# Optimization experiments

Measured on AMD Instinct MI355X. Metric: run time of the kernel, lower is better.

The kernel has to match this reference:

```python
import jax, jax.numpy as jnp
import numpy as np

B, H, S, DK = 2, 16, 2048, 128


def setup_inputs() -> dict:
    key = jax.random.key(0)
    kq, kk, kv = jax.random.split(key, 3)
    return {
        "queries": jax.random.normal(kq, (B, H, S, DK), dtype=jnp.float32),
        "keys": jax.random.normal(kk, (B, H, S, DK), dtype=jnp.float32),
        "values": jax.random.normal(kv, (B, H, S, DK), dtype=jnp.float32),
        "d_k": DK,
    }


def reference(queries, keys, values, d_k):
    # scores: [B, H, Sq, Sk] = Q @ K^T / sqrt(d_k)
    scale = 1.0 / np.sqrt(float(d_k)).astype(np.float32)
    scores = jnp.einsum("bhqd,bhkd->bhqk", queries, keys) * scale
    weights = jax.nn.softmax(scores, axis=-1)
    return jnp.einsum("bhqk,bhkd->bhqd", weights, values)
```

## Files before the change

kernel.cpp:

```cpp
#include <hip/hip_runtime.h>
#include <hip/hip_bf16.h>

#define SREF 2048
#define DHEAD 128
#define KVBLK 64
#define NTHREADS 256
#define ATHREADS 512
#define NT (SREF / KVBLK)
#define PSTR 72
#define QSCALE 0.12751743f
#define THRLOG 8.0f

typedef short bf16x8 __attribute__((ext_vector_type(8)));
typedef float f32x4 __attribute__((ext_vector_type(4)));
typedef float f32x16 __attribute__((ext_vector_type(16)));

typedef const __attribute__((address_space(1))) void* gas_t;
typedef __attribute__((address_space(3))) void* las_t;

__device__ __forceinline__ ushort f2bf(float x) {
    unsigned u = __builtin_bit_cast(unsigned, x);
    u += 0x7fffu + ((u >> 16) & 1u);
    return (ushort)(u >> 16);
}

__device__ __forceinline__ float fexp2(float x) {
#if __has_builtin(__builtin_amdgcn_exp2f)
    return __builtin_amdgcn_exp2f(x);
#else
    return exp2f(x);
#endif
}

__device__ __forceinline__ unsigned cvtpk(float lo, float hi) {
    unsigned r;
    asm("v_cvt_pk_bf16_f32 %0, %1, %2" : "=v"(r) : "v"(lo), "v"(hi));
    return r;
}

__global__ __launch_bounds__(NTHREADS) void preconv_kernel(
    const float* __restrict__ K, const float* __restrict__ V,
    ushort* __restrict__ Kb, ushort* __restrict__ VTb)
{
    __shared__ ushort T[DHEAD * PSTR];
    const int t  = threadIdx.x;
    const int bh = blockIdx.y;
    const int s0 = blockIdx.x * 64;
    const size_t base = (size_t)bh * SREF * DHEAD;

    const float* kb = K + base + (size_t)s0 * DHEAD;
    ushort* kout = Kb + base + (size_t)s0 * DHEAD;
    #pragma unroll
    for (int i = 0; i < 8; ++i) {
        int idx = t + i * NTHREADS;
        float4 f = *(const float4*)(kb + idx * 4);
        ushort4 h; h.x = f2bf(f.x); h.y = f2bf(f.y); h.z = f2bf(f.z); h.w = f2bf(f.w);
        *(ushort4*)(kout + idx * 4) = h;
    }

    const float* vb = V + base + (size_t)s0 * DHEAD;
    #pragma unroll
    for (int i = 0; i < 8; ++i) {
        const int key = (t & 31) + 32 * (i & 1);
        const int d4  = (t >> 5) + 8 * (i >> 1);
        float4 f = *(const float4*)(vb + key * DHEAD + d4 * 4);
        T[(d4 * 4 + 0) * PSTR + key] = f2bf(f.x);
        T[(d4 * 4 + 1) * PSTR + key] = f2bf(f.y);
        T[(d4 * 4 + 2) * PSTR + key] = f2bf(f.z);
        T[(d4 * 4 + 3) * PSTR + key] = f2bf(f.w);
    }
    __syncthreads();

    ushort* vt = VTb + (size_t)bh * DHEAD * SREF + s0;
    #pragma unroll
    for (int i = 0; i < 4; ++i) {
        int idx = t + i * NTHREADS;
        int d = idx >> 3;
        int c = (idx & 7) * 8;
        bf16x8 v = *(const bf16x8*)&T[d * PSTR + c];
        *(bf16x8*)(vt + (size_t)d * SREF + c) = v;
    }
}

__device__ __forceinline__ void softmax_step(
    f32x16& s0, f32x16& s1, float& mrun, float& lsumh,
    f32x16* acc, bf16x8* pa)
{
    float m0[8];
    #pragma unroll
    for (int i = 0; i < 8; ++i)
        m0[i] = fmaxf(fmaxf(s0[i], s0[i + 8]), fmaxf(s1[i], s1[i + 8]));
    float pmax = fmaxf(fmaxf(fmaxf(m0[0], m0[1]), fmaxf(m0[2], m0[3])),
                       fmaxf(fmaxf(m0[4], m0[5]), fmaxf(m0[6], m0[7])));
    pmax = fmaxf(pmax, __shfl_xor(pmax, 32));

    if (!__all(pmax <= mrun + THRLOG)) {
        const float mnew  = fmaxf(mrun, pmax);
        const float alpha = fexp2(mrun - mnew);
        mrun = mnew;
        lsumh *= alpha;
        #pragma unroll
        for (int db = 0; db < 4; ++db)
            #pragma unroll
            for (int i = 0; i < 16; ++i) acc[db][i] *= alpha;
    }

    float r0 = 0.f, r1 = 0.f, r2 = 0.f, r3 = 0.f;
    #pragma unroll
    for (int i = 0; i < 16; i += 4) {
        s0[i]   = fexp2(s0[i]   - mrun); r0 += s0[i];
        s0[i+1] = fexp2(s0[i+1] - mrun); r1 += s0[i+1];
        s0[i+2] = fexp2(s0[i+2] - mrun); r2 += s0[i+2];
        s0[i+3] = fexp2(s0[i+3] - mrun); r3 += s0[i+3];
    }
    #pragma unroll
    for (int i = 0; i < 16; i += 4) {
        s1[i]   = fexp2(s1[i]   - mrun); r0 += s1[i];
        s1[i+1] = fexp2(s1[i+1] - mrun); r1 += s1[i+1];
        s1[i+2] = fexp2(s1[i+2] - mrun); r2 += s1[i+2];
        s1[i+3] = fexp2(s1[i+3] - mrun); r3 += s1[i+3];
    }
    lsumh += (r0 + r1) + (r2 + r3);

    #pragma unroll
    for (int kb = 0; kb < 2; ++kb) {
        #pragma unroll
        for (int c = 0; c < 2; ++c) {
            unsigned x0, x1, y0, y1;
            if (kb == 0) {
                x0 = cvtpk(s0[8*c+0], s0[8*c+1]); x1 = cvtpk(s0[8*c+2], s0[8*c+3]);
                y0 = cvtpk(s0[8*c+4], s0[8*c+5]); y1 = cvtpk(s0[8*c+6], s0[8*c+7]);
            } else {
                x0 = cvtpk(s1[8*c+0], s1[8*c+1]); x1 = cvtpk(s1[8*c+2], s1[8*c+3]);
                y0 = cvtpk(s1[8*c+4], s1[8*c+5]); y1 = cvtpk(s1[8*c+6], s1[8*c+7]);
            }
            asm volatile("v_permlane32_swap_b32 %0, %1" : "+v"(x0), "+v"(y0));
            asm volatile("v_permlane32_swap_b32 %0, %1" : "+v"(x1), "+v"(y1));
            union { unsigned u[4]; bf16x8 v; } U;
            U.u[0] = x0; U.u[1] = x1; U.u[2] = y0; U.u[3] = y1;
            pa[kb * 2 + c] = U.v;
        }
    }
}

__global__ __launch_bounds__(ATHREADS, 2) void attn_fwd_kernel(
    const float* __restrict__ Q, const ushort* __restrict__ Kb,
    const ushort* __restrict__ VTb, float* __restrict__ O)
{
    __shared__ __align__(16) char smem[65536];

    const int t    = threadIdx.x;
    const int lane = t & 63;
    const int wv   = t >> 6;
    const int g    = wv >> 2;
    const int hi   = lane >> 5;
    const int q5   = lane & 31;
    const int sw   = (q5 & 15) << 4;

    const int bh = blockIdx.x;
    const int q0 = blockIdx.y * 256;
    const size_t base = (size_t)bh * SREF * DHEAD;

    bf16x8 qf[8];
    {
        const float* qrow = Q + base + (size_t)(q0 + wv * 32 + q5) * DHEAD;
        #pragma unroll
        for (int dk = 0; dk < 8; ++dk) {
            const int d0 = dk * 16 + hi * 8;
            float4 a = *(const float4*)(qrow + d0);
            float4 b = *(const float4*)(qrow + d0 + 4);
            bf16x8 f;
            f[0] = (short)f2bf(a.x * QSCALE); f[1] = (short)f2bf(a.y * QSCALE);
            f[2] = (short)f2bf(a.z * QSCALE); f[3] = (short)f2bf(a.w * QSCALE);
            f[4] = (short)f2bf(b.x * QSCALE); f[5] = (short)f2bf(b.y * QSCALE);
            f[6] = (short)f2bf(b.z * QSCALE); f[7] = (short)f2bf(b.w * QSCALE);
            qf[dk] = f;
        }
    }

    const char* ksrcb = (const char*)(Kb + base);
    const char* vsrcb = (const char*)(VTb + (size_t)bh * DHEAD * SREF);

    const int kread = q5 * 256 + ((hi * 16) ^ sw);
    const int vread = q5 * 256 + ((hi * 16) ^ sw);

#define STAGE_K(tt) do {                                                        \
    const char* kt_ = ksrcb + (size_t)(tt) * 16384;                             \
    _Pragma("unroll")                                                           \
    for (int i_ = 0; i_ < 2; ++i_) {                                            \
        int L_ = t * 16 + i_ * 8192;                                            \
        int r_ = L_ >> 8;                                                       \
        __builtin_amdgcn_global_load_lds(                                       \
            (gas_t)(const void*)(kt_ + (L_ ^ ((r_ & 15) << 4))),                \
            (las_t)(void*)(smem + ((tt) & 1) * 16384 + L_), 16, 0, 0);          \
    }                                                                           \
} while (0)

#define STAGE_V(tt) do {                                                        \
    const char* vt_ = vsrcb + (size_t)(tt) * 128;                               \
    _Pragma("unroll")                                                           \
    for (int i_ = 0; i_ < 2; ++i_) {                                            \
        int L_ = t * 16 + i_ * 8192;                                            \
        int r_ = L_ >> 8;                                                       \
        int offp_ = (L_ & 255) ^ ((r_ & 15) << 4);                              \
        int d_ = r_ + 64 * (offp_ >> 7);                                        \
        __builtin_amdgcn_global_load_lds(                                       \
            (gas_t)(const void*)(vt_ + (size_t)d_ * (SREF * 2) + (offp_ & 127)),\
            (las_t)(void*)(smem + 32768 + ((tt) & 1) * 16384 + L_), 16, 0, 0);  \
    }                                                                           \
} while (0)

#define QK(tt) do {                                                             \
    const int kO_ = ((tt) & 1) * 16384;                                         \
    _Pragma("unroll")                                                           \
    for (int i_ = 0; i_ < 16; ++i_) { s0[i_] = 0.f; s1[i_] = 0.f; }             \
    __builtin_amdgcn_s_setprio(1);                                              \
    _Pragma("unroll")                                                           \
    for (int dk_ = 0; dk_ < 8; ++dk_) {                                         \
        const int off_ = kread ^ (dk_ << 5);                                    \
        bf16x8 kf0 = *(const bf16x8*)(smem + kO_ + off_);                       \
        s0 = __builtin_amdgcn_mfma_f32_32x32x16_bf16(kf0, qf[dk_], s0, 0, 0, 0);\
        bf16x8 kf1 = *(const bf16x8*)(smem + kO_ + 8192 + off_);                \
        s1 = __builtin_amdgcn_mfma_f32_32x32x16_bf16(kf1, qf[dk_], s1, 0, 0, 0);\
    }                                                                           \
    __builtin_amdgcn_s_setprio(0);                                              \
} while (0)

#define PV(tt) do {                                                             \
    const int vO_ = 32768 + ((tt) & 1) * 16384;                                 \
    __builtin_amdgcn_s_setprio(1);                                              \
    _Pragma("unroll")                                                           \
    for (int db_ = 0; db_ < 4; ++db_) {                                         \
        const int vb_ = vread + (db_ & 1) * 8192;                               \
        _Pragma("unroll")                                                       \
        for (int ks_ = 0; ks_ < 4; ++ks_) {                                     \
            bf16x8 vf = *(const bf16x8*)(smem + vO_ +                           \
                (vb_ ^ (ks_ << 5) ^ ((db_ >> 1) << 7)));                        \
            acc[db_] = __builtin_amdgcn_mfma_f32_32x32x16_bf16(vf, pa[ks_], acc[db_], 0, 0, 0); \
        }                                                                       \
    }                                                                           \
    __builtin_amdgcn_s_setprio(0);                                              \
} while (0)

#define BAR() do { __builtin_amdgcn_s_barrier(); __builtin_amdgcn_sched_barrier(0); } while (0)

    float mrun = -1e30f, lsumh = 0.0f;
    f32x16 acc[4];
    #pragma unroll
    for (int db = 0; db < 4; ++db)
        #pragma unroll
        for (int i = 0; i < 16; ++i) acc[db][i] = 0.0f;

    f32x16 s0, s1;
    bf16x8 pa[4];

    STAGE_K(0);
    asm volatile("s_waitcnt vmcnt(0)" ::: "memory");
    BAR();

    STAGE_K(1);
    STAGE_V(0);
    if (g == 0) { QK(0); }
    BAR();
    if (g == 0) { softmax_step(s0, s1, mrun, lsumh, acc, pa); }
    else        { QK(0); }
    asm volatile("s_waitcnt vmcnt(0)" ::: "memory");
    BAR();

    #pragma unroll 1
    for (int tt = 1; tt < NT; ++tt) {
        if (tt + 1 < NT) STAGE_K(tt + 1);
        STAGE_V(tt);
        if (g == 0) { PV(tt - 1); QK(tt); }
        else        { softmax_step(s0, s1, mrun, lsumh, acc, pa); }
        BAR();
        if (g == 0) { softmax_step(s0, s1, mrun, lsumh, acc, pa); }
        else        { PV(tt - 1); QK(tt); }
        asm volatile("s_waitcnt vmcnt(0)" ::: "memory");
        BAR();
    }

    if (g == 0) { PV(NT - 1); }
    else        { softmax_step(s0, s1, mrun, lsumh, acc, pa); }
    BAR();
    if (g == 1) { PV(NT - 1); }

    __syncthreads();
    const float lsum = lsumh + __shfl_xor(lsumh, 32);
    const float inv  = 1.0f / lsum;

    #pragma unroll
    for (int round = 0; round < 3; ++round) {
        if (wv / 3 == round) {
            const int eb = (wv % 3) * 16896;
            #pragma unroll
            for (int db = 0; db < 4; ++db) {
                #pragma unroll
                for (int c = 0; c < 4; ++c) {
                    f32x4 v;
                    v[0] = acc[db][4*c+0] * inv;
                    v[1] = acc[db][4*c+1] * inv;
                    v[2] = acc[db][4*c+2] * inv;
                    v[3] = acc[db][4*c+3] * inv;
                    *(f32x4*)(smem + eb + q5 * 528 + db * 128 + c * 32 + hi * 16) = v;
                }
            }
            #pragma unroll
            for (int i = 0; i < 16; ++i) {
                const int flat  = lane + i * 64;
                const int row   = flat >> 5;
                const int chunk = flat & 31;
                f32x4 v = *(const f32x4*)(smem + eb + row * 528 + chunk * 16);
                *(f32x4*)(O + base + (size_t)(q0 + wv * 32 + row) * DHEAD + chunk * 4) = v;
            }
        }
        __syncthreads();
    }
#undef STAGE_K
#undef STAGE_V
#undef QK
#undef PV
#undef BAR
}

__global__ __launch_bounds__(NTHREADS) void attn_fwd_fallback(
    const float* __restrict__ Q, const float* __restrict__ K,
    const float* __restrict__ V, float* __restrict__ O)
{
    __shared__ ushort Ksh[64 * 136];
    __shared__ ushort Vsh[DHEAD * 72];
    __shared__ ushort Psh[4][16 * PSTR];

    const int t    = threadIdx.x;
    const int lane = t & 63;
    const int wv   = t >> 6;
    const int lq   = lane & 15;
    const int kh   = lane >> 4;

    const int bh = blockIdx.y;
    const int q0 = blockIdx.x * 64;
    const size_t base = (size_t)bh * SREF * DHEAD;

    const float scale = 0.08838834764831845f;
    bf16x8 qf[4];
    {
        const float* qrow = Q + base + (size_t)(q0 + wv * 16 + lq) * DHEAD;
        #pragma unroll
        for (int kk = 0; kk < 4; ++kk) {
            const int d0 = kk * 32 + kh * 8;
            float4 a = *(const float4*)(qrow + d0);
            float4 b = *(const float4*)(qrow + d0 + 4);
            bf16x8 f;
            f[0] = (short)f2bf(a.x * scale); f[1] = (short)f2bf(a.y * scale);
            f[2] = (short)f2bf(a.z * scale); f[3] = (short)f2bf(a.w * scale);
            f[4] = (short)f2bf(b.x * scale); f[5] = (short)f2bf(b.y * scale);
            f[6] = (short)f2bf(b.z * scale); f[7] = (short)f2bf(b.w * scale);
            qf[kk] = f;
        }
    }

    float mrun[4], lrun[4];
    f32x4 acc_o[8];
    #pragma unroll
    for (int r = 0; r < 4; ++r) { mrun[r] = -1e30f; lrun[r] = 0.0f; }
    #pragma unroll
    for (int db = 0; db < 8; ++db) acc_o[db] = (f32x4){0.f, 0.f, 0.f, 0.f};

    for (int kv0 = 0; kv0 < SREF; kv0 += 64) {
        __syncthreads();
        const float* kbase = K + base + (size_t)kv0 * DHEAD;
        #pragma unroll
        for (int i = 0; i < 8; ++i) {
            const int idx = t + i * NTHREADS;
            const int row = idx >> 5;
            const int c4  = idx & 31;
            float4 f = *(const float4*)(kbase + row * DHEAD + c4 * 4);
            ushort4 h;
            h.x = f2bf(f.x); h.y = f2bf(f.y); h.z = f2bf(f.z); h.w = f2bf(f.w);
            *(ushort4*)&Ksh[row * 136 + c4 * 4] = h;
        }
        const float* vbase = V + base + (size_t)kv0 * DHEAD;
        #pragma unroll
        for (int i = 0; i < 8; ++i) {
            const int key = (t & 31) + 32 * (i & 1);
            const int d4  = (t >> 5) + 8 * (i >> 1);
            float4 f = *(const float4*)(vbase + key * DHEAD + d4 * 4);
            Vsh[(d4 * 4 + 0) * 72 + key] = f2bf(f.x);
            Vsh[(d4 * 4 + 1) * 72 + key] = f2bf(f.y);
            Vsh[(d4 * 4 + 2) * 72 + key] = f2bf(f.z);
            Vsh[(d4 * 4 + 3) * 72 + key] = f2bf(f.w);
        }
        __syncthreads();

        f32x4 accs[4];
        #pragma unroll
        for (int nb = 0; nb < 4; ++nb) accs[nb] = (f32x4){0.f, 0.f, 0.f, 0.f};
        #pragma unroll
        for (int kk = 0; kk < 4; ++kk) {
            #pragma unroll
            for (int nb = 0; nb < 4; ++nb) {
                bf16x8 kf = *(const bf16x8*)&Ksh[(nb * 16 + lq) * 136 + kk * 32 + kh * 8];
                accs[nb] = __builtin_amdgcn_mfma_f32_16x16x32_bf16(qf[kk], kf, accs[nb], 0, 0, 0);
            }
        }

        float ps[4][4];
        #pragma unroll
        for (int r = 0; r < 4; ++r) {
            float v = fmaxf(fmaxf(accs[0][r], accs[1][r]), fmaxf(accs[2][r], accs[3][r]));
            #pragma unroll
            for (int mk = 1; mk < 16; mk <<= 1) v = fmaxf(v, __shfl_xor(v, mk));
            const float mnew  = fmaxf(mrun[r], v);
            const float alpha = __expf(mrun[r] - mnew);
            mrun[r] = mnew;
            float rs = 0.0f;
            #pragma unroll
            for (int nb = 0; nb < 4; ++nb) {
                const float p = __expf(accs[nb][r] - mnew);
                ps[nb][r] = p;
                rs += p;
            }
            #pragma unroll
            for (int mk = 1; mk < 16; mk <<= 1) rs += __shfl_xor(rs, mk);
            lrun[r] = lrun[r] * alpha + rs;
            #pragma unroll
            for (int db = 0; db < 8; ++db) acc_o[db][r] *= alpha;
        }

        #pragma unroll
        for (int nb = 0; nb < 4; ++nb)
            #pragma unroll
            for (int r = 0; r < 4; ++r)
                Psh[wv][(kh * 4 + r) * PSTR + nb * 16 + lq] = f2bf(ps[nb][r]);

        #pragma unroll
        for (int ks = 0; ks < 2; ++ks) {
            bf16x8 pa = *(const bf16x8*)&Psh[wv][lq * PSTR + ks * 32 + kh * 8];
            #pragma unroll
            for (int db = 0; db < 8; ++db) {
                bf16x8 vf = *(const bf16x8*)&Vsh[(db * 16 + lq) * 72 + ks * 32 + kh * 8];
                acc_o[db] = __builtin_amdgcn_mfma_f32_16x16x32_bf16(pa, vf, acc_o[db], 0, 0, 0);
            }
        }
    }

    #pragma unroll
    for (int r = 0; r < 4; ++r) {
        const float inv = 1.0f / lrun[r];
        float* orow = O + base + (size_t)(q0 + wv * 16 + kh * 4 + r) * DHEAD;
        #pragma unroll
        for (int db = 0; db < 8; ++db)
            orow[db * 16 + lq] = acc_o[db][r] * inv;
    }
}

extern "C" void kernel_launch(void* const* d_in, const int* in_sizes, int n_in,
                              void* d_out, int out_size, void* d_ws, size_t ws_size,
                              hipStream_t stream) {
    const float* Q = (const float*)d_in[0];
    const float* K = (const float*)d_in[1];
    const float* V = (const float*)d_in[2];
    float* O = (float*)d_out;
    const int BH = in_sizes[0] / (SREF * DHEAD);
    const size_t nel = (size_t)BH * SREF * DHEAD;

    if (ws_size >= 2 * nel * sizeof(ushort)) {
        ushort* Kb  = (ushort*)d_ws;
        ushort* VTb = Kb + nel;
        preconv_kernel<<<dim3(SREF / 64, BH), NTHREADS, 0, stream>>>(K, V, Kb, VTb);
        attn_fwd_kernel<<<dim3(BH, SREF / 256), ATHREADS, 0, stream>>>(Q, Kb, VTb, O);
    } else {
        attn_fwd_fallback<<<dim3(SREF / 64, BH), NTHREADS, 0, stream>>>(Q, K, V, O);
    }
}
```

Before: 98.59 us.

## Process two query tiles per wave with 256 threads, dropping ping-pong wave groups

Replaces the 512-thread design, where two 4-wave groups alternate QK/PV and softmax between barriers, with 4 waves that each own 64 query rows split into two 32-row tiles (A/B). Each K/V fragment read from LDS now feeds two MFMAs, halving LDS reads per FLOP. K and V staging is merged into one double-buffered stage with a partial vmcnt wait. The trade-off is the loss of cross-group overlap between softmax and matrix work, fewer waves per CU, and roughly double the accumulator register pressure.

```diff
diff --git a/kernel.cpp b/kernel.cpp
--- a/kernel.cpp
+++ b/kernel.cpp
@@ -5,7 +5,6 @@
 #define DHEAD 128
 #define KVBLK 64
 #define NTHREADS 256
-#define ATHREADS 512
 #define NT (SREF / KVBLK)
 #define PSTR 72
 #define QSCALE 0.12751743f
@@ -143,7 +142,7 @@
     }
 }
 
-__global__ __launch_bounds__(ATHREADS, 2) void attn_fwd_kernel(
+__global__ __launch_bounds__(NTHREADS, 1) void attn_fwd_kernel(
     const float* __restrict__ Q, const ushort* __restrict__ Kb,
     const ushort* __restrict__ VTb, float* __restrict__ O)
 {
@@ -152,7 +151,6 @@
     const int t    = threadIdx.x;
     const int lane = t & 63;
     const int wv   = t >> 6;
-    const int g    = wv >> 2;
     const int hi   = lane >> 5;
     const int q5   = lane & 31;
     const int sw   = (q5 & 15) << 4;
@@ -161,20 +159,29 @@
     const int q0 = blockIdx.y * 256;
     const size_t base = (size_t)bh * SREF * DHEAD;
 
-    bf16x8 qf[8];
+    bf16x8 qfA[8], qfB[8];
     {
-        const float* qrow = Q + base + (size_t)(q0 + wv * 32 + q5) * DHEAD;
+        const float* qrowA = Q + base + (size_t)(q0 + wv * 64 + q5) * DHEAD;
+        const float* qrowB = qrowA + 32 * DHEAD;
         #pragma unroll
         for (int dk = 0; dk < 8; ++dk) {
             const int d0 = dk * 16 + hi * 8;
-            float4 a = *(const float4*)(qrow + d0);
-            float4 b = *(const float4*)(qrow + d0 + 4);
+            float4 a = *(const float4*)(qrowA + d0);
+            float4 b = *(const float4*)(qrowA + d0 + 4);
             bf16x8 f;
             f[0] = (short)f2bf(a.x * QSCALE); f[1] = (short)f2bf(a.y * QSCALE);
             f[2] = (short)f2bf(a.z * QSCALE); f[3] = (short)f2bf(a.w * QSCALE);
             f[4] = (short)f2bf(b.x * QSCALE); f[5] = (short)f2bf(b.y * QSCALE);
             f[6] = (short)f2bf(b.z * QSCALE); f[7] = (short)f2bf(b.w * QSCALE);
-            qf[dk] = f;
+            qfA[dk] = f;
+            float4 c = *(const float4*)(qrowB + d0);
+            float4 d = *(const float4*)(qrowB + d0 + 4);
+            bf16x8 g;
+            g[0] = (short)f2bf(c.x * QSCALE); g[1] = (short)f2bf(c.y * QSCALE);
+            g[2] = (short)f2bf(c.z * QSCALE); g[3] = (short)f2bf(c.w * QSCALE);
+            g[4] = (short)f2bf(d.x * QSCALE); g[5] = (short)f2bf(d.y * QSCALE);
+            g[6] = (short)f2bf(d.z * QSCALE); g[7] = (short)f2bf(d.w * QSCALE);
+            qfB[dk] = g;
         }
     }
 
@@ -182,25 +189,22 @@
     const char* vsrcb = (const char*)(VTb + (size_t)bh * DHEAD * SREF);
 
     const int kread = q5 * 256 + ((hi * 16) ^ sw);
-    const int vread = q5 * 256 + ((hi * 16) ^ sw);
-
-#define STAGE_K(tt) do {                                                        \
+    const int vread = kread;
+
+#define STAGE(tt) do {                                                          \
     const char* kt_ = ksrcb + (size_t)(tt) * 16384;                             \
+    const char* vt_ = vsrcb + (size_t)(tt) * 128;                               \
     _Pragma("unroll")                                                           \
-    for (int i_ = 0; i_ < 2; ++i_) {                                            \
-        int L_ = t * 16 + i_ * 8192;                                            \
+    for (int i_ = 0; i_ < 4; ++i_) {                                            \
+        int L_ = t * 16 + i_ * 4096;                                            \
         int r_ = L_ >> 8;                                                       \
         __builtin_amdgcn_global_load_lds(                                       \
             (gas_t)(const void*)(kt_ + (L_ ^ ((r_ & 15) << 4))),                \
             (las_t)(void*)(smem + ((tt) & 1) * 16384 + L_), 16, 0, 0);          \
     }                                                                           \
-} while (0)
-
-#define STAGE_V(tt) do {                                                        \
-    const char* vt_ = vsrcb + (size_t)(tt) * 128;                               \
     _Pragma("unroll")                                                           \
-    for (int i_ = 0; i_ < 2; ++i_) {                                            \
-        int L_ = t * 16 + i_ * 8192;                                            \
+    for (int i_ = 0; i_ < 4; ++i_) {                                            \
+        int L_ = t * 16 + i_ * 4096;                                            \
         int r_ = L_ >> 8;                                                       \
         int offp_ = (L_ & 255) ^ ((r_ & 15) << 4);                              \
         int d_ = r_ + 64 * (offp_ >> 7);                                        \
@@ -210,117 +214,107 @@
     }                                                                           \
 } while (0)
 
-#define QK(tt) do {                                                             \
-    const int kO_ = ((tt) & 1) * 16384;                                         \
-    _Pragma("unroll")                                                           \
-    for (int i_ = 0; i_ < 16; ++i_) { s0[i_] = 0.f; s1[i_] = 0.f; }             \
-    __builtin_amdgcn_s_setprio(1);                                              \
-    _Pragma("unroll")                                                           \
-    for (int dk_ = 0; dk_ < 8; ++dk_) {                                         \
-        const int off_ = kread ^ (dk_ << 5);                                    \
-        bf16x8 kf0 = *(const bf16x8*)(smem + kO_ + off_);                       \
-        s0 = __builtin_amdgcn_mfma_f32_32x32x16_bf16(kf0, qf[dk_], s0, 0, 0, 0);\
-        bf16x8 kf1 = *(const bf16x8*)(smem + kO_ + 8192 + off_);                \
-        s1 = __builtin_amdgcn_mfma_f32_32x32x16_bf16(kf1, qf[dk_], s1, 0, 0, 0);\
-    }                                                                           \
-    __builtin_amdgcn_s_setprio(0);                                              \
-} while (0)
-
-#define PV(tt) do {                                                             \
-    const int vO_ = 32768 + ((tt) & 1) * 16384;                                 \
-    __builtin_amdgcn_s_setprio(1);                                              \
-    _Pragma("unroll")                                                           \
-    for (int db_ = 0; db_ < 4; ++db_) {                                         \
-        const int vb_ = vread + (db_ & 1) * 8192;                               \
-        _Pragma("unroll")                                                       \
-        for (int ks_ = 0; ks_ < 4; ++ks_) {                                     \
-            bf16x8 vf = *(const bf16x8*)(smem + vO_ +                           \
-                (vb_ ^ (ks_ << 5) ^ ((db_ >> 1) << 7)));                        \
-            acc[db_] = __builtin_amdgcn_mfma_f32_32x32x16_bf16(vf, pa[ks_], acc[db_], 0, 0, 0); \
-        }                                                                       \
-    }                                                                           \
-    __builtin_amdgcn_s_setprio(0);                                              \
-} while (0)
-
-#define BAR() do { __builtin_amdgcn_s_barrier(); __builtin_amdgcn_sched_barrier(0); } while (0)
-
-    float mrun = -1e30f, lsumh = 0.0f;
-    f32x16 acc[4];
+    float mrunA = -1e30f, lsumA = 0.0f;
+    float mrunB = -1e30f, lsumB = 0.0f;
+    f32x16 accA[4], accB[4];
     #pragma unroll
     for (int db = 0; db < 4; ++db)
         #pragma unroll
-        for (int i = 0; i < 16; ++i) acc[db][i] = 0.0f;
-
-    f32x16 s0, s1;
-    bf16x8 pa[4];
-
-    STAGE_K(0);
-    asm volatile("s_waitcnt vmcnt(0)" ::: "memory");
-    BAR();
-
-    STAGE_K(1);
-    STAGE_V(0);
-    if (g == 0) { QK(0); }
-    BAR();
-    if (g == 0) { softmax_step(s0, s1, mrun, lsumh, acc, pa); }
-    else        { QK(0); }
-    asm volatile("s_waitcnt vmcnt(0)" ::: "memory");
-    BAR();
+        for (int i = 0; i < 16; ++i) { accA[db][i] = 0.0f; accB[db][i] = 0.0f; }
+
+    f32x16 sA0, sA1, sB0, sB1;
+    bf16x8 paA[4], paB[4];
+
+    STAGE(0);
 
     #pragma unroll 1
-    for (int tt = 1; tt < NT; ++tt) {
-        if (tt + 1 < NT) STAGE_K(tt + 1);
-        STAGE_V(tt);
-        if (g == 0) { PV(tt - 1); QK(tt); }
-        else        { softmax_step(s0, s1, mrun, lsumh, acc, pa); }
-        BAR();
-        if (g == 0) { softmax_step(s0, s1, mrun, lsumh, acc, pa); }
-        else        { PV(tt - 1); QK(tt); }
-        asm volatile("s_waitcnt vmcnt(0)" ::: "memory");
-        BAR();
-    }
-
-    if (g == 0) { PV(NT - 1); }
-    else        { softmax_step(s0, s1, mrun, lsumh, acc, pa); }
-    BAR();
-    if (g == 1) { PV(NT - 1); }
+    for (int tt = 0; tt < NT; ++tt) {
+        if (tt + 1 < NT) {
+            STAGE(tt + 1);
+            asm volatile("s_waitcnt vmcnt(8)" ::: "memory");
+        } else {
+            asm volatile("s_waitcnt vmcnt(0)" ::: "memory");
+        }
+        __builtin_amdgcn_s_barrier();
+        __builtin_amdgcn_sched_barrier(0);
+
+        const int kO = ((tt) & 1) * 16384;
+        const int vO = 32768 + ((tt) & 1) * 16384;
+
+        #pragma unroll
+        for (int i = 0; i < 16; ++i) { sA0[i] = 0.f; sA1[i] = 0.f; sB0[i] = 0.f; sB1[i] = 0.f; }
+        #pragma unroll
+        for (int dk = 0; dk < 8; ++dk) {
+            const int off = kread ^ (dk << 5);
+            bf16x8 kf0 = *(const bf16x8*)(smem + kO + off);
+            bf16x8 kf1 = *(const bf16x8*)(smem + kO + 8192 + off);
+            sA0 = __builtin_amdgcn_mfma_f32_32x32x16_bf16(kf0, qfA[dk], sA0, 0, 0, 0);
+            sB0 = __builtin_amdgcn_mfma_f32_32x32x16_bf16(kf0, qfB[dk], sB0, 0, 0, 0);
+            sA1 = __builtin_amdgcn_mfma_f32_32x32x16_bf16(kf1, qfA[dk], sA1, 0, 0, 0);
+            sB1 = __builtin_amdgcn_mfma_f32_32x32x16_bf16(kf1, qfB[dk], sB1, 0, 0, 0);
+        }
+
+        softmax_step(sA0, sA1, mrunA, lsumA, accA, paA);
+        softmax_step(sB0, sB1, mrunB, lsumB, accB, paB);
+
+        #pragma unroll
+        for (int db = 0; db < 4; ++db) {
+            const int vb = vread + (db & 1) * 8192;
+            #pragma unroll
+            for (int ks = 0; ks < 4; ++ks) {
+                bf16x8 vf = *(const bf16x8*)(smem + vO +
+                    (vb ^ (ks << 5) ^ ((db >> 1) << 7)));
+                accA[db] = __builtin_amdgcn_mfma_f32_32x32x16_bf16(vf, paA[ks], accA[db], 0, 0, 0);
+                accB[db] = __builtin_amdgcn_mfma_f32_32x32x16_bf16(vf, paB[ks], accB[db], 0, 0, 0);
+            }
+        }
+
+        __builtin_amdgcn_sched_barrier(0);
+        __builtin_amdgcn_s_barrier();
+    }
 
     __syncthreads();
-    const float lsum = lsumh + __shfl_xor(lsumh, 32);
-    const float inv  = 1.0f / lsum;
-
-    #pragma unroll
-    for (int round = 0; round < 3; ++round) {
-        if (wv / 3 == round) {
-            const int eb = (wv % 3) * 16896;
-            #pragma unroll
-            for (int db = 0; db < 4; ++db) {
+    const float lA = lsumA + __shfl_xor(lsumA, 32);
+    const float lB = lsumB + __shfl_xor(lsumB, 32);
+    const float invA = 1.0f / lA;
+    const float invB = 1.0f / lB;
+
+    #pragma unroll
+    for (int round = 0; round < 2; ++round) {
+        if ((wv >> 1) == round) {
+            const int eb = (wv & 1) * 16896;
+            #pragma unroll
+            for (int g = 0; g < 2; ++g) {
+                const float inv = g ? invB : invA;
                 #pragma unroll
-                for (int c = 0; c < 4; ++c) {
-                    f32x4 v;
-                    v[0] = acc[db][4*c+0] * inv;
-                    v[1] = acc[db][4*c+1] * inv;
-                    v[2] = acc[db][4*c+2] * inv;
-                    v[3] = acc[db][4*c+3] * inv;
-                    *(f32x4*)(smem + eb + q5 * 528 + db * 128 + c * 32 + hi * 16) = v;
+                for (int db = 0; db < 4; ++db) {
+                    #pragma unroll
+                    for (int c = 0; c < 4; ++c) {
+                        f32x4 v;
+                        if (g) {
+                            v[0] = accB[db][4*c+0] * inv; v[1] = accB[db][4*c+1] * inv;
+                            v[2] = accB[db][4*c+2] * inv; v[3] = accB[db][4*c+3] * inv;
+                        } else {
+                            v[0] = accA[db][4*c+0] * inv; v[1] = accA[db][4*c+1] * inv;
+                            v[2] = accA[db][4*c+2] * inv; v[3] = accA[db][4*c+3] * inv;
+                        }
+                        *(f32x4*)(smem + eb + q5 * 528 + db * 128 + c * 32 + hi * 16) = v;
+                    }
                 }
-            }
-            #pragma unroll
-            for (int i = 0; i < 16; ++i) {
-                const int flat  = lane + i * 64;
-                const int row   = flat >> 5;
-                const int chunk = flat & 31;
-                f32x4 v = *(const f32x4*)(smem + eb + row * 528 + chunk * 16);
-                *(f32x4*)(O + base + (size_t)(q0 + wv * 32 + row) * DHEAD + chunk * 4) = v;
+                #pragma unroll
+                for (int i = 0; i < 16; ++i) {
+                    const int flat  = lane + i * 64;
+                    const int row   = flat >> 5;
+                    const int chunk = flat & 31;
+                    f32x4 v = *(const f32x4*)(smem + eb + row * 528 + chunk * 16);
+                    *(f32x4*)(O + base +
+                        (size_t)(q0 + wv * 64 + g * 32 + row) * DHEAD + chunk * 4) = v;
+                }
             }
         }
         __syncthreads();
     }
-#undef STAGE_K
-#undef STAGE_V
-#undef QK
-#undef PV
-#undef BAR
+#undef STAGE
 }
 
 __global__ __launch_bounds__(NTHREADS) void attn_fwd_fallback(
@@ -468,7 +462,7 @@
         ushort* Kb  = (ushort*)d_ws;
         ushort* VTb = Kb + nel;
         preconv_kernel<<<dim3(SREF / 64, BH), NTHREADS, 0, stream>>>(K, V, Kb, VTb);
-        attn_fwd_kernel<<<dim3(BH, SREF / 256), ATHREADS, 0, stream>>>(Q, Kb, VTb, O);
+        attn_fwd_kernel<<<dim3(BH, SREF / 256), NTHREADS, 0, stream>>>(Q, Kb, VTb, O);
     } else {
         attn_fwd_fallback<<<dim3(SREF / 64, BH), NTHREADS, 0, stream>>>(Q, K, V, O);
     }
```

Measured after the change: 115.9 us. +17.6%, slower.
